# Optimization experiments

Measured on AMD Instinct MI355X. Metric: run time of the kernel, lower is better.

## Reference

```python
import jax, jax.numpy as jnp
import numpy as np

N = 20000      # nodes
E = 320000     # edges (avg degree 16)
D = 256        # embedding_dim
H = 8          # num_heads
DH = D // H    # head_dim = 32
ED = 64        # edge_dim
FF = 4 * D     # feed-forward hidden
EPS = 1e-5


def setup_inputs() -> dict:
    key = jax.random.key(0)
    ks = jax.random.split(key, 32)

    def lin_w(k, i, o):
        return (jax.random.normal(k, (i, o), jnp.float32) / np.sqrt(i)).astype(jnp.float32)

    return {
        "x": jax.random.normal(ks[0], (N, D), jnp.float32),
        "edge_features": jax.random.normal(ks[1], (E, ED), jnp.float32),
        "edge_weights": jax.random.uniform(ks[2], (E,), jnp.float32),
        "edge_index": jax.random.randint(ks[3], (2, E), 0, N, dtype=jnp.int32),
        "Wq": lin_w(ks[4], D, D), "bq": jnp.zeros((D,), jnp.float32),
        "Wk": lin_w(ks[5], D, D), "bk": jnp.zeros((D,), jnp.float32),
        "Wv": lin_w(ks[6], D, D), "bv": jnp.zeros((D,), jnp.float32),
        "We": lin_w(ks[7], ED, DH), "be": jnp.zeros((DH,), jnp.float32),
        "Wo": lin_w(ks[8], D, D), "bo": jnp.zeros((D,), jnp.float32),
        "ln1_g": jnp.ones((D,), jnp.float32), "ln1_b": jnp.zeros((D,), jnp.float32),
        "ln2_g": jnp.ones((D,), jnp.float32), "ln2_b": jnp.zeros((D,), jnp.float32),
        "W1": lin_w(ks[9], D, FF), "b1": jnp.zeros((FF,), jnp.float32),
        "W2": lin_w(ks[10], FF, D), "b2": jnp.zeros((D,), jnp.float32),
        "alpha": jnp.ones((1,), jnp.float32),
        "beta": jnp.ones((1,), jnp.float32),
    }


def _layernorm(x, g, b):
    m = jnp.mean(x, axis=-1, keepdims=True)
    v = jnp.var(x, axis=-1, keepdims=True)
    return (x - m) * jax.lax.rsqrt(v + EPS) * g + b


def _edge_attention(xn, edge_index, ef, ew, Wq, bq, Wk, bk, Wv, bv, We, be, Wo, bo):
    n = xn.shape[0]
    scale = DH ** -0.5
    q = (xn @ Wq + bq).reshape(n, H, DH)
    k = (xn @ Wk + bk).reshape(n, H, DH)
    v = (xn @ Wv + bv).reshape(n, H, DH)
    src, dst = edge_index[0], edge_index[1]
    ep = ef @ We + be                               # [E, DH], shared across heads
    # per-edge, per-head scores: q[dst] . (k[src] + edge_proj)
    scores = jnp.einsum('ehd,ehd->eh', q[dst], k[src] + ep[:, None, :]) * scale
    scores = scores * ew[:, None]
    # segment softmax over incoming edges of each dst node
    m = jax.ops.segment_max(scores, dst, num_segments=n)
    m = jnp.where(jnp.isfinite(m), m, 0.0)          # nodes with no incoming edges
    ex = jnp.exp(scores - m[dst])
    s = jax.ops.segment_sum(ex, dst, num_segments=n)
    attn = ex / s[dst]                              # [E, H]
    # scatter-weighted V aggregation; nodes with no edges stay zero (matches torch)
    out = jax.ops.segment_sum(attn[:, :, None] * v[src], dst, num_segments=n)
    out = out.reshape(n, D) @ Wo + bo
    return out


def reference(x, edge_features, edge_weights, edge_index,
              Wq, bq, Wk, bk, Wv, bv, We, be, Wo, bo,
              ln1_g, ln1_b, ln2_g, ln2_b, W1, b1, W2, b2, alpha, beta):
    xn = _layernorm(x, ln1_g, ln1_b)
    attn_out = _edge_attention(xn, edge_index, edge_features, edge_weights,
                               Wq, bq, Wk, bk, Wv, bv, We, be, Wo, bo)
    x = x + alpha * attn_out
    xn = _layernorm(x, ln2_g, ln2_b)
    ff = jax.nn.gelu(xn @ W1 + b1, approximate=False) @ W2 + b2
    x = x + beta * ff
    return x
```

## Files before the change

### kernel.cpp

```cpp
#include <hip/hip_runtime.h>
#include <math.h>

#define NN 20000
#define EE 320000
#define DD 256
#define HH 8
#define DHD 32
#define EDF 64
#define FFD 1024

typedef unsigned short u16;
typedef __attribute__((ext_vector_type(8))) __bf16 bf16x8;
typedef __attribute__((ext_vector_type(8))) unsigned short u16x8;
typedef __attribute__((ext_vector_type(4))) float f32x4;

#define XN_OFF   (0)
#define AGGB_OFF (2560000)
#define X1_OFF   (5120000)
#define QKV_OFF  (10240000)
#define EP_OFF   (25600000)
#define WT_OFF   (35840000)
#define BQKV_OFF (36240000)
#define CSR_OFF  (36250000)

__device__ __forceinline__ u16 f2bf(float f) {
    unsigned u = __float_as_uint(f);
    return (u16)((u + 0x7FFFu + ((u >> 16) & 1u)) >> 16);
}
__device__ __forceinline__ float bf2f(u16 h) {
    return __uint_as_float(((unsigned)h) << 16);
}
__device__ __forceinline__ float gelu_exact(float v) {
    return 0.5f * v * (1.0f + erff(v * 0.70710678118654752f));
}

#define GLDS16(g, l) __builtin_amdgcn_global_load_lds(             \
    (__attribute__((address_space(1))) void*)(g),                  \
    (__attribute__((address_space(3))) void*)(l), 16, 0, 0)

__device__ __forceinline__ void ln_body(const float* __restrict__ x,
                                        const float* __restrict__ g,
                                        const float* __restrict__ b,
                                        u16* __restrict__ out, int vb) {
    int row = vb * 4 + (threadIdx.x >> 6);
    if (row >= NN) return;
    int lane = threadIdx.x & 63;
    float4 v = *(const float4*)&x[(size_t)row * DD + lane * 4];
    float s  = v.x + v.y + v.z + v.w;
    float ss = v.x * v.x + v.y * v.y + v.z * v.z + v.w * v.w;
    #pragma unroll
    for (int o = 32; o >= 1; o >>= 1) {
        s  += __shfl_xor(s, o);
        ss += __shfl_xor(ss, o);
    }
    float mean = s * (1.0f / DD);
    float var  = ss * (1.0f / DD) - mean * mean;
    float inv  = rsqrtf(var + 1e-5f);
    float4 gg = *(const float4*)&g[lane * 4];
    float4 bb = *(const float4*)&b[lane * 4];
    ushort4 o4;
    o4.x = f2bf((v.x - mean) * inv * gg.x + bb.x);
    o4.y = f2bf((v.y - mean) * inv * gg.y + bb.y);
    o4.z = f2bf((v.z - mean) * inv * gg.z + bb.z);
    o4.w = f2bf((v.w - mean) * inv * gg.w + bb.w);
    *(ushort4*)&out[(size_t)row * DD + lane * 4] = o4;
}

__global__ __launch_bounds__(256) void ln_kernel(const float* __restrict__ x,
                                                 const float* __restrict__ g,
                                                 const float* __restrict__ b,
                                                 u16* __restrict__ out) {
    ln_body(x, g, b, out, blockIdx.x);
}

__device__ __forceinline__ void convw_body(const float* __restrict__ src,
                                           u16* __restrict__ dst, int K, int N,
                                           int vb) {
    int n = vb * 4 + (threadIdx.x >> 6);
    int lane = threadIdx.x & 63;
    if (n >= N) return;
    for (int k = lane * 4; k < K; k += 256) {
        ushort4 o;
        o.x = f2bf(src[(size_t)(k + 0) * N + n]);
        o.y = f2bf(src[(size_t)(k + 1) * N + n]);
        o.z = f2bf(src[(size_t)(k + 2) * N + n]);
        o.w = f2bf(src[(size_t)(k + 3) * N + n]);
        *(ushort4*)&dst[(size_t)n * K + k] = o;
    }
}

__global__ __launch_bounds__(256) void prep_count_ln_kernel(
    const float* __restrict__ Wq, const float* __restrict__ Wk,
    const float* __restrict__ Wv, const float* __restrict__ Wo,
    const float* __restrict__ W1, const float* __restrict__ W2,
    const float* __restrict__ We,
    const float* __restrict__ bq, const float* __restrict__ bk,
    const float* __restrict__ bv,
    u16* __restrict__ WqkvT, u16* __restrict__ WoT, u16* __restrict__ W1T,
    u16* __restrict__ W2T, u16* __restrict__ WeT, float* __restrict__ bqkv,
    const int* __restrict__ ei, int* __restrict__ counts,
    const float* __restrict__ x, const float* __restrict__ ln1g,
    const float* __restrict__ ln1b, u16* __restrict__ xn) {
    int b = blockIdx.x;
    if      (b < 64)  convw_body(Wq, WqkvT,            256, 256,  b);
    else if (b < 128) convw_body(Wk, WqkvT + 65536,    256, 256,  b - 64);
    else if (b < 192) convw_body(Wv, WqkvT + 131072,   256, 256,  b - 128);
    else if (b < 256) convw_body(Wo, WoT,              256, 256,  b - 192);
    else if (b < 512) convw_body(W1, W1T,              256, 1024, b - 256);
    else if (b < 576) convw_body(W2, W2T,              1024, 256, b - 512);
    else if (b < 584) convw_body(We, WeT,              64,  32,   b - 576);
    else if (b < 585) {
        int t = threadIdx.x;
        bqkv[t] = bq[t];
        bqkv[256 + t] = bk[t];
        bqkv[512 + t] = bv[t];
    } else if (b < 1835) {
        int e = (b - 585) * 256 + threadIdx.x;
        if (e < EE) atomicAdd(&counts[ei[EE + e]], 1);
    } else {
        ln_body(x, ln1g, ln1b, xn, b - 1835);
    }
}

template <int BM, int BN, int EPI>
__device__ __forceinline__ void gemm_body(
    const u16* __restrict__ A, const u16* __restrict__ BT,
    const float* __restrict__ bias,
    float* __restrict__ Cf, u16* __restrict__ Cb,
    const float* __restrict__ res, const float* __restrict__ scale,
    int M, int K, int N, int bxx, int byy)
{
    constexpr int FM = BM / 32, FN = BN / 32;
    constexpr int nA = BM / 32, nB = BN / 32;
    constexpr int NST = (nA > nB) ? nA : nB;
    __shared__ u16 Asm[BM * 64];
    __shared__ u16 Bsm[BN * 64];
    const int tid  = threadIdx.x;
    const int lane = tid & 63;
    const int w    = tid >> 6;
    const int wr   = w >> 1, wc = w & 1;
    const int bm   = bxx * BM;
    const int bn   = byy * BN;

    f32x4 acc[FM][FN] = {};

    int st_row[NST], st_src[NST], st_dst[NST];
    #pragma unroll
    for (int i = 0; i < NST; i++) {
        int base  = i * 4096 + w * 1024;
        int off   = base + lane * 16;
        int row   = off >> 7;
        int inner = off & 127;
        st_row[i] = row;
        st_src[i] = (inner ^ ((row & 7) << 4)) >> 1;
        st_dst[i] = base;
    }
    const int arow0 = wr * (BM / 2) + (lane & 15);
    const int brow0 = wc * (BN / 2) + (lane & 15);
    const int kb0   = (lane >> 4) * 16;

    for (int k0 = 0; k0 < K; k0 += 64) {
        #pragma unroll
        for (int i = 0; i < nA; i++) {
            int r = bm + st_row[i]; if (r > M - 1) r = M - 1;
            GLDS16(A + (size_t)r * K + k0 + st_src[i], (char*)Asm + st_dst[i]);
        }
        #pragma unroll
        for (int i = 0; i < nB; i++) {
            int r = bn + st_row[i];
            GLDS16(BT + (size_t)r * K + k0 + st_src[i], (char*)Bsm + st_dst[i]);
        }
        asm volatile("s_waitcnt vmcnt(0)" ::: "memory");
        __syncthreads();
        #pragma unroll
        for (int s = 0; s < 2; s++) {
            bf16x8 af[FM], bfv[FN];
            #pragma unroll
            for (int i = 0; i < FM; i++) {
                int row  = arow0 + i * 16;
                int byte = (row << 7) + ((kb0 + s * 64) ^ ((row & 7) << 4));
                af[i] = *(const bf16x8*)((const char*)Asm + byte);
            }
            #pragma unroll
            for (int j = 0; j < FN; j++) {
                int row  = brow0 + j * 16;
                int byte = (row << 7) + ((kb0 + s * 64) ^ ((row & 7) << 4));
                bfv[j] = *(const bf16x8*)((const char*)Bsm + byte);
            }
            #pragma unroll
            for (int i = 0; i < FM; i++)
                #pragma unroll
                for (int j = 0; j < FN; j++)
                    acc[i][j] = __builtin_amdgcn_mfma_f32_16x16x32_bf16(
                        af[i], bfv[j], acc[i][j], 0, 0, 0);
        }
        __syncthreads();
    }

    float sc = 0.f;
    if constexpr (EPI == 2) sc = scale[0];
    const int col0 = bn + wc * (BN / 2) + (lane & 15);
    const int row0 = bm + wr * (BM / 2) + ((lane >> 4) << 2);
    #pragma unroll
    for (int i = 0; i < FM; i++) {
        #pragma unroll
        for (int j = 0; j < FN; j++) {
            int col = col0 + j * 16;
            float bb = bias[col];
            #pragma unroll
            for (int r = 0; r < 4; r++) {
                int row = row0 + i * 16 + r;
                if (row < M) {
                    float o = acc[i][j][r] + bb;
                    if constexpr (EPI == 1) {
                        Cb[(size_t)row * N + col] = f2bf(gelu_exact(o));
                    } else if constexpr (EPI == 2) {
                        Cf[(size_t)row * N + col] = res[(size_t)row * N + col] + sc * o;
                    } else if constexpr (EPI == 3) {
                        if (col < 256) {
                            Cb[(size_t)row * 256 + col] = f2bf(o * 0.17677669529663689f);
                        } else if (col < 512) {
                            Cb[(size_t)NN * 256 + (size_t)row * 512 + (col - 256) * 2] = f2bf(o);
                        } else {
                            Cb[(size_t)NN * 256 + (size_t)row * 512 + (col - 512) * 2 + 1] = f2bf(o);
                        }
                    } else {
                        Cf[(size_t)row * N + col] = o;
                    }
                }
            }
        }
    }
}

template <int BM, int BN, int EPI>
__global__ __launch_bounds__(256) void gemm_bf16(
    const u16* __restrict__ A, const u16* __restrict__ BT,
    const float* __restrict__ bias,
    float* __restrict__ Cf, u16* __restrict__ Cb,
    const float* __restrict__ res, const float* __restrict__ scale,
    int M, int K, int N) {
    gemm_body<BM, BN, EPI>(A, BT, bias, Cf, Cb, res, scale, M, K, N,
                           blockIdx.x, blockIdx.y);
}

__device__ __forceinline__ void ep_body(const float* __restrict__ ef,
                                        const u16* __restrict__ WeT,
                                        const float* __restrict__ be,
                                        const int* __restrict__ epos,
                                        u16* __restrict__ epc, int blk) {
    const int lane = threadIdx.x & 63;
    const int wv   = threadIdx.x >> 6;
    const int e0   = blk * 64 + wv * 16;
    const int ar   = lane & 15;
    const int k8   = (lane >> 4) * 8;

    f32x4 acc[2] = {};
    #pragma unroll
    for (int s = 0; s < 2; s++) {
        const float* ap = ef + (size_t)(e0 + ar) * EDF + s * 32 + k8;
        float4 a0 = *(const float4*)ap;
        float4 a1 = *(const float4*)(ap + 4);
        bf16x8 af;
        af[0] = (__bf16)a0.x; af[1] = (__bf16)a0.y; af[2] = (__bf16)a0.z; af[3] = (__bf16)a0.w;
        af[4] = (__bf16)a1.x; af[5] = (__bf16)a1.y; af[6] = (__bf16)a1.z; af[7] = (__bf16)a1.w;
        #pragma unroll
        for (int j = 0; j < 2; j++) {
            bf16x8 bf = *(const bf16x8*)&WeT[(size_t)(j * 16 + ar) * EDF + s * 32 + k8];
            acc[j] = __builtin_amdgcn_mfma_f32_16x16x32_bf16(af, bf, acc[j], 0, 0, 0);
        }
    }
    const int row0 = (lane >> 4) << 2;
    #pragma unroll
    for (int r = 0; r < 4; r++) {
        int pos = epos[e0 + row0 + r];
        #pragma unroll
        for (int j = 0; j < 2; j++) {
            int col = j * 16 + ar;
            epc[(size_t)pos * DHD + col] = f2bf(acc[j][r] + be[col]);
        }
    }
}

__global__ __launch_bounds__(256) void qkv_ep_kernel(
    const u16* __restrict__ xn, const u16* __restrict__ WqkvT,
    const float* __restrict__ bqkv, u16* __restrict__ qb,
    const float* __restrict__ ef, const u16* __restrict__ WeT,
    const float* __restrict__ be, const int* __restrict__ epos,
    u16* __restrict__ epc) {
    int b = blockIdx.x;
    if (b < 942) {
        gemm_body<128, 128, 3>(xn, WqkvT, bqkv, nullptr, qb, nullptr, nullptr,
                               NN, DD, 768, b % 157, b / 157);
    } else {
        ep_body(ef, WeT, be, epos, epc, b - 942);
    }
}

__global__ __launch_bounds__(1024) void scan_kernel(const int* __restrict__ counts,
                                                    int* __restrict__ row_start,
                                                    int* __restrict__ cursor) {
    __shared__ int part[1024];
    const int CH = 20;
    int t = threadIdx.x;
    int base = t * CH;
    int loc[CH];
    int s = 0;
    #pragma unroll
    for (int i = 0; i < CH; i++) {
        int idx = base + i;
        int c = (idx < NN) ? counts[idx] : 0;
        loc[i] = s;
        s += c;
    }
    part[t] = s;
    __syncthreads();
    for (int o = 1; o < 1024; o <<= 1) {
        int vv = (t >= o) ? part[t - o] : 0;
        __syncthreads();
        part[t] += vv;
        __syncthreads();
    }
    int off = (t > 0) ? part[t - 1] : 0;
    #pragma unroll
    for (int i = 0; i < CH; i++) {
        int idx = base + i;
        if (idx < NN) {
            int rs = off + loc[i];
            row_start[idx] = rs;
            cursor[idx] = rs;
        }
    }
    if (t == 1023) row_start[NN] = part[1023];
}

__global__ __launch_bounds__(256) void fill_kernel(const int* __restrict__ ei,
                                                   const float* __restrict__ ew,
                                                   int* __restrict__ cursor,
                                                   int2* __restrict__ csr,
                                                   int* __restrict__ epos) {
    int e = blockIdx.x * 256 + threadIdx.x;
    if (e >= EE) return;
    int src = ei[e];
    int dst = ei[EE + e];
    int pos = atomicAdd(&cursor[dst], 1);
    csr[pos] = make_int2(src, __float_as_int(ew[e] * 1.44269504088896f));
    epos[e] = pos;
}

__global__ __launch_bounds__(256) void attn_kernel(const u16* __restrict__ qb,
                                                   const u16* __restrict__ kv,
                                                   const u16* __restrict__ epc,
                                                   const int2* __restrict__ csr,
                                                   const int* __restrict__ row_start,
                                                   u16* __restrict__ aggb) {
    const int dst  = blockIdx.x * 4 + (threadIdx.x >> 6);
    const int lane = threadIdx.x & 63;
    const int g    = lane & 7;
    const int d0   = (lane >> 3) * 32 + g * 4;
    const int beg = row_start[dst];
    const int end = row_start[dst + 1];
    ushort4 q4 = *(const ushort4*)&qb[(size_t)dst * DD + d0];
    float4 qv = make_float4(bf2f(q4.x), bf2f(q4.y), bf2f(q4.z), bf2f(q4.w));
    float ss = 0.f;
    float4 acc = make_float4(0.f, 0.f, 0.f, 0.f);

    int i = beg;
    if ((i & 1) && i < end) {
        int2 p = csr[i];
        u16x8 kk = *(const u16x8*)&kv[(size_t)p.x * 512 + d0 * 2];
        ushort4 e4 = *(const ushort4*)&epc[(size_t)i * DHD + g * 4];
        float k0 = bf2f(kk[0]) + bf2f(e4.x);
        float k1 = bf2f(kk[2]) + bf2f(e4.y);
        float k2 = bf2f(kk[4]) + bf2f(e4.z);
        float k3 = bf2f(kk[6]) + bf2f(e4.w);
        float pv = fmaf(qv.x, k0, fmaf(qv.y, k1, fmaf(qv.z, k2, qv.w * k3)));
        #pragma unroll
        for (int o = 4; o >= 1; o >>= 1) pv += __shfl_xor(pv, o);
        float wq = exp2f(pv * __int_as_float(p.y));
        ss += wq;
        acc.x = fmaf(wq, bf2f(kk[1]), acc.x);
        acc.y = fmaf(wq, bf2f(kk[3]), acc.y);
        acc.z = fmaf(wq, bf2f(kk[5]), acc.z);
        acc.w = fmaf(wq, bf2f(kk[7]), acc.w);
        ++i;
    }
    for (; i + 4 <= end; i += 4) {
        int4 c01 = *(const int4*)&csr[i];
        int4 c23 = *(const int4*)&csr[i + 2];
        int   sr[4] = {c01.x, c01.z, c23.x, c23.z};
        float wt[4] = {__int_as_float(c01.y), __int_as_float(c01.w),
                       __int_as_float(c23.y), __int_as_float(c23.w)};
        u16x8 kk[4];
        ushort4 e4[4];
        #pragma unroll
        for (int u = 0; u < 4; u++) {
            kk[u] = *(const u16x8*)&kv[(size_t)sr[u] * 512 + d0 * 2];
            e4[u] = *(const ushort4*)&epc[(size_t)(i + u) * DHD + g * 4];
        }
        float pp[4];
        #pragma unroll
        for (int u = 0; u < 4; u++) {
            float k0 = bf2f(kk[u][0]) + bf2f(e4[u].x);
            float k1 = bf2f(kk[u][2]) + bf2f(e4[u].y);
            float k2 = bf2f(kk[u][4]) + bf2f(e4[u].z);
            float k3 = bf2f(kk[u][6]) + bf2f(e4[u].w);
            pp[u] = fmaf(qv.x, k0, fmaf(qv.y, k1, fmaf(qv.z, k2, qv.w * k3)));
        }
        #pragma unroll
        for (int o = 4; o >= 1; o >>= 1) {
            #pragma unroll
            for (int u = 0; u < 4; u++) pp[u] += __shfl_xor(pp[u], o);
        }
        #pragma unroll
        for (int u = 0; u < 4; u++) {
            float wq = exp2f(pp[u] * wt[u]);
            ss += wq;
            acc.x = fmaf(wq, bf2f(kk[u][1]), acc.x);
            acc.y = fmaf(wq, bf2f(kk[u][3]), acc.y);
            acc.z = fmaf(wq, bf2f(kk[u][5]), acc.z);
            acc.w = fmaf(wq, bf2f(kk[u][7]), acc.w);
        }
    }
    for (; i < end; ++i) {
        int2 p = csr[i];
        u16x8 kk = *(const u16x8*)&kv[(size_t)p.x * 512 + d0 * 2];
        ushort4 e4 = *(const ushort4*)&epc[(size_t)i * DHD + g * 4];
        float k0 = bf2f(kk[0]) + bf2f(e4.x);
        float k1 = bf2f(kk[2]) + bf2f(e4.y);
        float k2 = bf2f(kk[4]) + bf2f(e4.z);
        float k3 = bf2f(kk[6]) + bf2f(e4.w);
        float pv = fmaf(qv.x, k0, fmaf(qv.y, k1, fmaf(qv.z, k2, qv.w * k3)));
        #pragma unroll
        for (int o = 4; o >= 1; o >>= 1) pv += __shfl_xor(pv, o);
        float wq = exp2f(pv * __int_as_float(p.y));
        ss += wq;
        acc.x = fmaf(wq, bf2f(kk[1]), acc.x);
        acc.y = fmaf(wq, bf2f(kk[3]), acc.y);
        acc.z = fmaf(wq, bf2f(kk[5]), acc.z);
        acc.w = fmaf(wq, bf2f(kk[7]), acc.w);
    }
    float inv = (end > beg) ? 1.f / ss : 0.f;
    ushort4 o4;
    o4.x = f2bf(acc.x * inv);
    o4.y = f2bf(acc.y * inv);
    o4.z = f2bf(acc.z * inv);
    o4.w = f2bf(acc.w * inv);
    *(ushort4*)&aggb[(size_t)dst * DD + d0] = o4;
}

extern "C" void kernel_launch(void* const* d_in, const int* in_sizes, int n_in,
                              void* d_out, int out_size, void* d_ws, size_t ws_size,
                              hipStream_t stream) {
    const float* x    = (const float*)d_in[0];
    const float* ef   = (const float*)d_in[1];
    const float* ew   = (const float*)d_in[2];
    const int*   ei   = (const int*)d_in[3];
    const float* Wq   = (const float*)d_in[4];
    const float* bq   = (const float*)d_in[5];
    const float* Wk   = (const float*)d_in[6];
    const float* bk   = (const float*)d_in[7];
    const float* Wv   = (const float*)d_in[8];
    const float* bv   = (const float*)d_in[9];
    const float* We   = (const float*)d_in[10];
    const float* be   = (const float*)d_in[11];
    const float* Wo   = (const float*)d_in[12];
    const float* bo   = (const float*)d_in[13];
    const float* ln1g = (const float*)d_in[14];
    const float* ln1b = (const float*)d_in[15];
    const float* ln2g = (const float*)d_in[16];
    const float* ln2b = (const float*)d_in[17];
    const float* W1   = (const float*)d_in[18];
    const float* b1   = (const float*)d_in[19];
    const float* W2   = (const float*)d_in[20];
    const float* b2   = (const float*)d_in[21];
    const float* alpha = (const float*)d_in[22];
    const float* beta  = (const float*)d_in[23];

    float* ws    = (float*)d_ws;
    u16*   xn    = (u16*)(ws + XN_OFF);
    u16*   aggb  = (u16*)(ws + AGGB_OFF);
    float* x1    = ws + X1_OFF;
    u16*   qb    = (u16*)(ws + QKV_OFF);
    u16*   kv    = qb + (size_t)NN * 256;
    u16*   ff1   = (u16*)(ws + QKV_OFF);
    u16*   epc   = (u16*)(ws + EP_OFF);
    u16*   wt    = (u16*)(ws + WT_OFF);
    u16*   WqkvT = wt;
    u16*   WoT   = wt + 768 * 256;
    u16*   W1T   = WoT + 256 * 256;
    u16*   W2T   = W1T + 1024 * 256;
    u16*   WeT   = W2T + 256 * 1024;
    float* bqkv  = ws + BQKV_OFF;
    float* out   = (float*)d_out;

    int*  counts    = (int*)(ws + CSR_OFF);
    int*  row_start = counts + NN;
    int*  cursor    = row_start + NN + 1;
    int2* csr       = (int2*)(counts + 60004);
    int*  epos      = counts + 60004 + 2 * EE;

    hipMemsetAsync(counts, 0, (size_t)NN * sizeof(int), stream);

    prep_count_ln_kernel<<<6835, 256, 0, stream>>>(
        Wq, Wk, Wv, Wo, W1, W2, We, bq, bk, bv,
        WqkvT, WoT, W1T, W2T, WeT, bqkv, ei, counts, x, ln1g, ln1b, xn);

    scan_kernel<<<1, 1024, 0, stream>>>(counts, row_start, cursor);
    fill_kernel<<<EE / 256, 256, 0, stream>>>(ei, ew, cursor, csr, epos);

    qkv_ep_kernel<<<5942, 256, 0, stream>>>(xn, WqkvT, bqkv, qb,
                                            ef, WeT, be, epos, epc);

    attn_kernel<<<NN / 4, 256, 0, stream>>>(qb, kv, epc, csr, row_start, aggb);

    gemm_bf16<64, 128, 2><<<dim3(313, 2), 256, 0, stream>>>(
        aggb, WoT, bo, x1, nullptr, x, alpha, NN, DD, DD);

    ln_kernel<<<NN / 4, 256, 0, stream>>>(x1, ln2g, ln2b, xn);

    gemm_bf16<128, 128, 1><<<dim3(157, 8), 256, 0, stream>>>(
        xn, W1T, b1, nullptr, ff1, nullptr, nullptr, NN, DD, FFD);
    gemm_bf16<64, 128, 2><<<dim3(313, 2), 256, 0, stream>>>(
        ff1, W2T, b2, out, nullptr, x1, beta, NN, FFD, DD);
}
```

Before: 269.9 us.

## Tile weight transposes via shared memory and stage edge features with async LDS loads

```diff
diff --git a/kernel.cpp b/kernel.cpp
--- a/kernel.cpp
+++ b/kernel.cpp
@@ -73,19 +73,32 @@
     ln_body(x, g, b, out, blockIdx.x);
 }
 
-__device__ __forceinline__ void convw_body(const float* __restrict__ src,
-                                           u16* __restrict__ dst, int K, int N,
-                                           int vb) {
-    int n = vb * 4 + (threadIdx.x >> 6);
-    int lane = threadIdx.x & 63;
-    if (n >= N) return;
-    for (int k = lane * 4; k < K; k += 256) {
-        ushort4 o;
-        o.x = f2bf(src[(size_t)(k + 0) * N + n]);
-        o.y = f2bf(src[(size_t)(k + 1) * N + n]);
-        o.z = f2bf(src[(size_t)(k + 2) * N + n]);
-        o.w = f2bf(src[(size_t)(k + 3) * N + n]);
-        *(ushort4*)&dst[(size_t)n * K + k] = o;
+__device__ __forceinline__ void transp_body(const float* __restrict__ src,
+                                            u16* __restrict__ dst,
+                                            int K, int N, int k0, int n0) {
+    __shared__ float Ws[64][65];
+    int t = threadIdx.x;
+    int rr = t >> 4, cc = (t & 15) * 4;
+    if (n0 + cc < N) {
+        #pragma unroll
+        for (int p = 0; p < 4; p++) {
+            int k = rr + p * 16;
+            float4 v = *(const float4*)&src[(size_t)(k0 + k) * N + n0 + cc];
+            Ws[k][cc + 0] = v.x; Ws[k][cc + 1] = v.y;
+            Ws[k][cc + 2] = v.z; Ws[k][cc + 3] = v.w;
+        }
+    }
+    __syncthreads();
+    int n = t >> 2, kc = (t & 3) * 16;
+    if (n0 + n < N) {
+        u16 o[16];
+        #pragma unroll
+        for (int j = 0; j < 16; j++) o[j] = f2bf(Ws[kc + j][n]);
+        u16* dp = dst + (size_t)(n0 + n) * K + k0 + kc;
+        *(ushort4*)(dp + 0)  = *(ushort4*)&o[0];
+        *(ushort4*)(dp + 4)  = *(ushort4*)&o[4];
+        *(ushort4*)(dp + 8)  = *(ushort4*)&o[8];
+        *(ushort4*)(dp + 12) = *(ushort4*)&o[12];
     }
 }
 
@@ -102,28 +115,34 @@
     const float* __restrict__ x, const float* __restrict__ ln1g,
     const float* __restrict__ ln1b, u16* __restrict__ xn) {
     int b = blockIdx.x;
-    if      (b < 64)  convw_body(Wq, WqkvT,            256, 256,  b);
-    else if (b < 128) convw_body(Wk, WqkvT + 65536,    256, 256,  b - 64);
-    else if (b < 192) convw_body(Wv, WqkvT + 131072,   256, 256,  b - 128);
-    else if (b < 256) convw_body(Wo, WoT,              256, 256,  b - 192);
-    else if (b < 512) convw_body(W1, W1T,              256, 1024, b - 256);
-    else if (b < 576) convw_body(W2, W2T,              1024, 256, b - 512);
-    else if (b < 584) convw_body(We, WeT,              64,  32,   b - 576);
-    else if (b < 585) {
+    if (b < 193) {
+        const float* src; u16* dst; int K, N, ti;
+        if      (b < 16)  { src = Wq; dst = WqkvT;          K = 256;  N = 256;  ti = b; }
+        else if (b < 32)  { src = Wk; dst = WqkvT + 65536;  K = 256;  N = 256;  ti = b - 16; }
+        else if (b < 48)  { src = Wv; dst = WqkvT + 131072; K = 256;  N = 256;  ti = b - 32; }
+        else if (b < 64)  { src = Wo; dst = WoT;            K = 256;  N = 256;  ti = b - 48; }
+        else if (b < 128) { src = W1; dst = W1T;            K = 256;  N = 1024; ti = b - 64; }
+        else if (b < 192) { src = W2; dst = W2T;            K = 1024; N = 256;  ti = b - 128; }
+        else              { src = We; dst = WeT;            K = 64;   N = 32;   ti = 0; }
+        int ntn = N >> 6; if (ntn == 0) ntn = 1;
+        int tk = ti / ntn, tn = ti % ntn;
+        transp_body(src, dst, K, N, tk * 64, tn * 64);
+    } else if (b == 193) {
         int t = threadIdx.x;
         bqkv[t] = bq[t];
         bqkv[256 + t] = bk[t];
         bqkv[512 + t] = bv[t];
-    } else if (b < 1835) {
-        int e = (b - 585) * 256 + threadIdx.x;
+    } else if (b < 1444) {
+        int e = (b - 194) * 256 + threadIdx.x;
         if (e < EE) atomicAdd(&counts[ei[EE + e]], 1);
     } else {
-        ln_body(x, ln1g, ln1b, xn, b - 1835);
+        ln_body(x, ln1g, ln1b, xn, b - 1444);
     }
 }
 
 template <int BM, int BN, int EPI>
 __device__ __forceinline__ void gemm_body(
+    char* smem,
     const u16* __restrict__ A, const u16* __restrict__ BT,
     const float* __restrict__ bias,
     float* __restrict__ Cf, u16* __restrict__ Cb,
@@ -133,8 +152,8 @@
     constexpr int FM = BM / 32, FN = BN / 32;
     constexpr int nA = BM / 32, nB = BN / 32;
     constexpr int NST = (nA > nB) ? nA : nB;
-    __shared__ u16 Asm[BM * 64];
-    __shared__ u16 Bsm[BN * 64];
+    u16* Asm = (u16*)smem;
+    u16* Bsm = (u16*)(smem + BM * 64 * 2);
     const int tid  = threadIdx.x;
     const int lane = tid & 63;
     const int w    = tid >> 6;
@@ -240,44 +259,62 @@
     float* __restrict__ Cf, u16* __restrict__ Cb,
     const float* __restrict__ res, const float* __restrict__ scale,
     int M, int K, int N) {
-    gemm_body<BM, BN, EPI>(A, BT, bias, Cf, Cb, res, scale, M, K, N,
+    __shared__ char smem[(BM + BN) * 64 * 2];
+    gemm_body<BM, BN, EPI>(smem, A, BT, bias, Cf, Cb, res, scale, M, K, N,
                            blockIdx.x, blockIdx.y);
 }
 
-__device__ __forceinline__ void ep_body(const float* __restrict__ ef,
+__device__ __forceinline__ void ep_body(char* smem,
+                                        const float* __restrict__ ef,
                                         const u16* __restrict__ WeT,
                                         const float* __restrict__ be,
                                         const int* __restrict__ epos,
                                         u16* __restrict__ epc, int blk) {
-    const int lane = threadIdx.x & 63;
-    const int wv   = threadIdx.x >> 6;
-    const int e0   = blk * 64 + wv * 16;
-    const int ar   = lane & 15;
-    const int k8   = (lane >> 4) * 8;
+    const int tid  = threadIdx.x;
+    const int lane = tid & 63;
+    const int w    = tid >> 6;
+    const int e0b  = blk * 64;
+
+    #pragma unroll
+    for (int j = 0; j < 4; j++) {
+        int gidx = (w * 4 + j) * 64 + lane;
+        int e    = gidx >> 4;
+        int cs   = (gidx & 15) << 4;
+        int c    = cs ^ ((e & 15) << 4);
+        GLDS16((const char*)ef + (size_t)(e0b + e) * 256 + c,
+               smem + (w * 4 + j) * 1024);
+    }
+    asm volatile("s_waitcnt vmcnt(0)" ::: "memory");
+    __syncthreads();
+
+    const int ar = lane & 15;
+    const int r  = w * 16 + ar;
+    const int e0 = e0b + w * 16;
 
     f32x4 acc[2] = {};
     #pragma unroll
     for (int s = 0; s < 2; s++) {
-        const float* ap = ef + (size_t)(e0 + ar) * EDF + s * 32 + k8;
-        float4 a0 = *(const float4*)ap;
-        float4 a1 = *(const float4*)(ap + 4);
+        int cbyte = (lane >> 4) * 32 + s * 128;
+        const char* base = smem + r * 256;
+        float4 a0 = *(const float4*)(base + ((cbyte)      ^ (ar << 4)));
+        float4 a1 = *(const float4*)(base + ((cbyte + 16) ^ (ar << 4)));
         bf16x8 af;
         af[0] = (__bf16)a0.x; af[1] = (__bf16)a0.y; af[2] = (__bf16)a0.z; af[3] = (__bf16)a0.w;
         af[4] = (__bf16)a1.x; af[5] = (__bf16)a1.y; af[6] = (__bf16)a1.z; af[7] = (__bf16)a1.w;
         #pragma unroll
         for (int j = 0; j < 2; j++) {
-            bf16x8 bf = *(const bf16x8*)&WeT[(size_t)(j * 16 + ar) * EDF + s * 32 + k8];
+            bf16x8 bf = *(const bf16x8*)&WeT[(size_t)(j * 16 + ar) * EDF + s * 32 + ((lane >> 4) * 8)];
             acc[j] = __builtin_amdgcn_mfma_f32_16x16x32_bf16(af, bf, acc[j], 0, 0, 0);
         }
     }
     const int row0 = (lane >> 4) << 2;
     #pragma unroll
-    for (int r = 0; r < 4; r++) {
-        int pos = epos[e0 + row0 + r];
+    for (int rr = 0; rr < 4; rr++) {
+        int pos = epos[e0 + row0 + rr];
         #pragma unroll
         for (int j = 0; j < 2; j++) {
             int col = j * 16 + ar;
-            epc[(size_t)pos * DHD + col] = f2bf(acc[j][r] + be[col]);
+            epc[(size_t)pos * DHD + col] = f2bf(acc[j][rr] + be[col]);
         }
     }
 }
@@ -288,12 +325,13 @@
     const float* __restrict__ ef, const u16* __restrict__ WeT,
     const float* __restrict__ be, const int* __restrict__ epos,
     u16* __restrict__ epc) {
+    __shared__ char smem[32768];
     int b = blockIdx.x;
     if (b < 942) {
-        gemm_body<128, 128, 3>(xn, WqkvT, bqkv, nullptr, qb, nullptr, nullptr,
-                               NN, DD, 768, b % 157, b / 157);
+        gemm_body<128, 128, 3>(smem, xn, WqkvT, bqkv, nullptr, qb, nullptr,
+                               nullptr, NN, DD, 768, b % 157, b / 157);
     } else {
-        ep_body(ef, WeT, be, epos, epc, b - 942);
+        ep_body(smem, ef, WeT, be, epos, epc, b - 942);
     }
 }
 
@@ -502,7 +540,7 @@
 
     hipMemsetAsync(counts, 0, (size_t)NN * sizeof(int), stream);
 
-    prep_count_ln_kernel<<<6835, 256, 0, stream>>>(
+    prep_count_ln_kernel<<<6444, 256, 0, stream>>>(
         Wq, Wk, Wv, Wo, W1, W2, We, bq, bk, bv,
         WqkvT, WoT, W1T, W2T, WeT, bqkv, ei, counts, x, ln1g, ln1b, xn);
 
```

New measurement: 263.9 us. 1.02x faster.
